# Optimization experiments

Hardware: AMD Instinct MI355X
Metric: run time of the kernel (lower is better)

The kernel has to match this reference:

```python
import jax, jax.numpy as jnp
import numpy as np

J0 = -0.1
J1 = 0.1
ALPHA = 0.15
BUMP_WIDTH_FACTOR = 10.0


def _w_delta7(n):
    idx = jnp.arange(n, dtype=jnp.float32)
    angle_diff = 2.0 * jnp.pi * (idx[:, None] - idx[None, :]) / n
    return jnp.cos(angle_diff)  # [N, N]


def _initial_bump(batch_size, n):
    # initial angle = pi for every batch element (matches r_init=None path)
    angles = jnp.full((batch_size,), jnp.pi, dtype=jnp.float32)
    centers = (angles * n / (2.0 * jnp.pi))[:, None]          # [B, 1]
    width = n / BUMP_WIDTH_FACTOR
    idx = jnp.arange(n, dtype=jnp.float32)[None, :]            # [1, N]
    d = jnp.abs(idx - centers)
    dist = jnp.minimum(d, n - d)                               # circular distance
    bump = jnp.exp(-(dist ** 2) / (2.0 * width ** 2))
    return bump / jnp.linalg.norm(bump, axis=1, keepdims=True)  # [B, N]


def setup_inputs() -> dict:
    key = jax.random.key(0)
    k1, k2, k3 = jax.random.split(key, 3)
    B, S, A, N = 64, 256, 32, 256
    action_signal = jax.random.normal(k1, (B, S, A), dtype=jnp.float32)
    Wo = jax.random.normal(k2, (N, N), dtype=jnp.float32) / np.sqrt(N)
    Wa = jax.random.normal(k3, (A, N, N), dtype=jnp.float32) / np.sqrt(N)
    return {"action_signal": action_signal, "Wo": Wo, "Wa": Wa}


def reference(action_signal, Wo, Wa):
    B, S, A = action_signal.shape
    N = Wo.shape[0]
    W_delta7 = _w_delta7(N)
    r0 = _initial_bump(B, N)
    # static part of the effective weight matrix: J1*W_delta7 + Wo
    W_static = J1 * W_delta7 + Wo  # [N, N]

    def step(r, a_t):
        # a_t: [B, A], r: [B, N]
        # W_eff = J0 + W_static + sum_a a_t[a]*Wa[a]; rec = W_eff @ r (per batch)
        Wa_weighted = jnp.einsum('ba,anm->bnm', a_t, Wa)       # [B, N, N]
        rec = (J0 * jnp.sum(r, axis=-1, keepdims=True)
               + r @ W_static.T
               + jnp.einsum('bnm,bm->bn', Wa_weighted, r))      # [B, N]
        r_new = (1.0 - ALPHA) * r + ALPHA * jax.nn.relu(rec)
        return r_new, r_new

    _, bumps = jax.lax.scan(step, r0, jnp.swapaxes(action_signal, 0, 1))
    bump_history = jnp.swapaxes(bumps, 0, 1)                   # [B, S, N]
    r_delta7 = bump_history @ W_delta7                          # [B, S, N]
    r_history = r_delta7 / jnp.max(r_delta7, axis=2, keepdims=True)
    return r_history, bump_history
```

## Files before the change

### kernel.cpp

```cpp
#include <hip/hip_runtime.h>
#include <math.h>

#define N_    256
#define B_    64
#define S_    256
#define A_    32
#define NSZ   8
#define BSZ   8
#define AROWS 33
#define LROWS 18
#define RROWS 15
#define ATS   12
#define J0_   (-0.1f)
#define J1_   (0.1f)
#define ALPHA_ 0.15f
#define WIDTH_ 25.6f
#define TWO_PI 6.283185307179586f

#define RPAR      (BSZ * N_)
#define RGRP      (2 * RPAR)
#define FLAG_OFF  (8 * RGRP)

#define WA_LDS_FLOATS (NSZ * LROWS * N_)
#define AT_LDS_FLOATS (2 * AROWS * ATS)
#define RLDS_FLOATS   (RPAR)
#define LDS_BYTES ((WA_LDS_FLOATS + AT_LDS_FLOATS + RLDS_FLOATS) * 4)

#define NN ((size_t)N_ * N_)

#define LOADX4_COH(dst, p) \
  asm volatile("global_load_dwordx4 %0, %1, off sc0 sc1" \
               : "=v"(dst) : "v"(p) : "memory")
#define LOADX4(dst, p) \
  asm volatile("global_load_dwordx4 %0, %1, off" : "=v"(dst) : "v"(p) : "memory")
#define WAIT_VM0() asm volatile("s_waitcnt vmcnt(0)" ::: "memory")

#define ROWFMA(wvec, a_idx) do {                                              \
    const float* atp_ = atb + (a_idx) * ATS;                                  \
    const float4 t0_ = *reinterpret_cast<const float4*>(atp_);                \
    const float4 t1_ = *reinterpret_cast<const float4*>(atp_ + 4);            \
    const float at8_[8] = {t0_.x,t0_.y,t0_.z,t0_.w,t1_.x,t1_.y,t1_.z,t1_.w};  \
    _Pragma("unroll")                                                         \
    for (int b_ = 0; b_ < 8; ++b_) {                                          \
      const float dd_ = (wvec).x*rr[b_][0] + (wvec).y*rr[b_][1] +             \
                        (wvec).z*rr[b_][2] + (wvec).w*rr[b_][3];              \
      acc[b_] += at8_[b_] * dd_;                                              \
    }                                                                         \
  } while (0)

__device__ __forceinline__ float bumpval(float idx) {
  float d = fabsf(idx - 128.0f);
  d = fminf(d, 256.0f - d);
  return expf(-d * d / (2.0f * WIDTH_ * WIDTH_));
}

__global__ __launch_bounds__(512, 1)
void ring_scan_kernel(const float* __restrict__ action,
                      const float* __restrict__ Wo,
                      const float* __restrict__ Wa,
                      float* __restrict__ out,
                      float* __restrict__ rws)
{
  extern __shared__ float lds[];
  float* wa_lds = lds;
  float* at_lds = lds + WA_LDS_FLOATS;
  float* r_lds  = lds + WA_LDS_FLOATS + AT_LDS_FLOATS;

  const int tid  = threadIdx.x;
  const int bid  = blockIdx.x;
  const int grp  = bid & 7;
  const int rank = bid >> 3;
  const int b0   = grp * BSZ;
  const int n0   = rank * NSZ;
  float*    rbase = rws + grp * RGRP;
  unsigned* flags = reinterpret_cast<unsigned*>(rws + FLAG_OFF) + grp * 32;

  for (int c = tid; c < NSZ * LROWS * (N_ / 4); c += 512) {
    const int rl = c >> 6;
    const int q  = c & 63;
    const int nl = rl / LROWS;
    const int a  = rl - nl * LROWS;
    const int n  = n0 + nl;
    float4 v;
    if (a < 17) {
      v = *reinterpret_cast<const float4*>(Wa + ((size_t)a * N_ + n) * N_ + q * 4);
    } else {
      const float4 wo = *reinterpret_cast<const float4*>(Wo + (size_t)n * N_ + q * 4);
      const float* wof = reinterpret_cast<const float*>(&wo);
      float tmp[4];
#pragma unroll
      for (int j = 0; j < 4; ++j) {
        const int m = q * 4 + j;
        tmp[j] = J0_ + J1_ * cosf((float)(n - m) * (TWO_PI / N_)) + wof[j];
      }
      v = make_float4(tmp[0], tmp[1], tmp[2], tmp[3]);
    }
    *reinterpret_cast<float4*>(wa_lds + rl * N_ + q * 4) = v;
  }
  if (tid < 16)
    at_lds[(tid >> 3) * (AROWS * ATS) + A_ * ATS + (tid & 7)] = 1.0f;
  if (tid < 256) {
    const int b = tid >> 5, a = tid & 31;
    at_lds[a * ATS + b] = action[((size_t)(b0 + b) * S_) * A_ + a];
  }

  const int wv = tid >> 6;
  const int mq = tid & 63;
  const int nG = n0 + wv;
  const float* wrow = wa_lds + wv * (LROWS * N_);
  const size_t bump_base = (size_t)B_ * S_ * N_;

  float4 sw0,sw1,sw2,sw3,sw4,sw5,sw6,sw7,sw8,sw9,sw10,sw11,sw12,sw13,sw14;
  {
    const float* wg = Wa + ((size_t)17 * N_ + nG) * N_ + mq * 4;
    LOADX4(sw0,  wg);           LOADX4(sw1,  wg + 1*NN);
    LOADX4(sw2,  wg + 2*NN);    LOADX4(sw3,  wg + 3*NN);
    LOADX4(sw4,  wg + 4*NN);    LOADX4(sw5,  wg + 5*NN);
    LOADX4(sw6,  wg + 6*NN);    LOADX4(sw7,  wg + 7*NN);
    LOADX4(sw8,  wg + 8*NN);    LOADX4(sw9,  wg + 9*NN);
    LOADX4(sw10, wg + 10*NN);   LOADX4(sw11, wg + 11*NN);
    LOADX4(sw12, wg + 12*NN);   LOADX4(sw13, wg + 13*NN);
    LOADX4(sw14, wg + 14*NN);
  }

  float g[4]; float ss = 0.0f;
#pragma unroll
  for (int j = 0; j < 4; ++j) { g[j] = bumpval((float)(mq * 4 + j)); ss += g[j] * g[j]; }
#pragma unroll
  for (int off = 1; off < 64; off <<= 1) ss += __shfl_xor(ss, off, 64);
  const float inv_norm = 1.0f / sqrtf(ss);

  float rr[8][4];
#pragma unroll
  for (int b = 0; b < 8; ++b)
#pragma unroll
    for (int j = 0; j < 4; ++j) rr[b][j] = g[j] * inv_norm;
  float rprev = (mq < 8) ? bumpval((float)nG) * inv_norm : 0.0f;

  __syncthreads();
  WAIT_VM0();

  for (int t = 0; t < S_; ++t) {
    const float* atb = at_lds + (t & 1) * (AROWS * ATS);

    if (t > 0) {
      const float* rsrc = rbase + ((t - 1) & 1) * RPAR;
      float4 rq;
      LOADX4_COH(rq, rsrc + tid * 4);
      WAIT_VM0();
      __builtin_amdgcn_sched_barrier(0);
      *reinterpret_cast<float4*>(r_lds + tid * 4) = rq;
      __syncthreads();
#pragma unroll
      for (int b = 0; b < 8; ++b) {
        const float4 rb = *reinterpret_cast<const float4*>(r_lds + b * N_ + mq * 4);
        rr[b][0] = rb.x; rr[b][1] = rb.y; rr[b][2] = rb.z; rr[b][3] = rb.w;
      }
    }

    float acc[8];
#pragma unroll
    for (int b = 0; b < 8; ++b) acc[b] = 0.0f;

#pragma unroll
    for (int a = 0; a < LROWS; ++a) {
      const float4 w = *reinterpret_cast<const float4*>(wrow + a * N_ + mq * 4);
      ROWFMA(w, (a < 17) ? a : 32);
    }
    ROWFMA(sw0, 17);  ROWFMA(sw1, 18);  ROWFMA(sw2, 19);  ROWFMA(sw3, 20);
    ROWFMA(sw4, 21);  ROWFMA(sw5, 22);  ROWFMA(sw6, 23);  ROWFMA(sw7, 24);
    ROWFMA(sw8, 25);  ROWFMA(sw9, 26);  ROWFMA(sw10, 27); ROWFMA(sw11, 28);
    ROWFMA(sw12, 29); ROWFMA(sw13, 30); ROWFMA(sw14, 31);

    const int bit0 = mq & 1, bit1 = mq & 2, bit2 = mq & 4;
    float t0 = bit0 ? acc[1] : acc[0], s0 = bit0 ? acc[0] : acc[1];
    float t1 = bit0 ? acc[3] : acc[2], s1 = bit0 ? acc[2] : acc[3];
    float t2 = bit0 ? acc[5] : acc[4], s2 = bit0 ? acc[4] : acc[5];
    float t3 = bit0 ? acc[7] : acc[6], s3 = bit0 ? acc[6] : acc[7];
    const float u0 = t0 + __shfl_xor(s0, 1, 64);
    const float u1 = t1 + __shfl_xor(s1, 1, 64);
    const float u2 = t2 + __shfl_xor(s2, 1, 64);
    const float u3 = t3 + __shfl_xor(s3, 1, 64);
    const float p0 = bit1 ? u1 : u0, q0 = bit1 ? u0 : u1;
    const float p1 = bit1 ? u3 : u2, q1 = bit1 ? u2 : u3;
    const float m0 = p0 + __shfl_xor(q0, 2, 64);
    const float m1 = p1 + __shfl_xor(q1, 2, 64);
    const float f0 = bit2 ? m1 : m0, g0 = bit2 ? m0 : m1;
    float f = f0 + __shfl_xor(g0, 4, 64);
    f += __shfl_xor(f, 8, 64);
    f += __shfl_xor(f, 16, 64);
    f += __shfl_xor(f, 32, 64);

    float rnew = 0.0f;
    if (mq < 8) {
      rnew = (1.0f - ALPHA_) * rprev + ALPHA_ * fmaxf(f, 0.0f);
      rprev = rnew;
      __hip_atomic_store(rbase + (t & 1) * RPAR + mq * N_ + nG, rnew,
                         __ATOMIC_RELAXED, __HIP_MEMORY_SCOPE_AGENT);
    }

    if (t == S_ - 1) {
      if (mq < 8)
        out[bump_base + ((size_t)(b0 + mq) * S_ + t) * N_ + nG] = rnew;
      break;
    }

    WAIT_VM0();
    __syncthreads();
    if (tid == 0)
      __hip_atomic_store(&flags[rank], (unsigned)(t + 1),
                         __ATOMIC_RELAXED, __HIP_MEMORY_SCOPE_AGENT);

    if (mq < 8)
      out[bump_base + ((size_t)(b0 + mq) * S_ + t) * N_ + nG] = rnew;
    if (tid < 256) {
      const int b = tid >> 5, a = tid & 31;
      at_lds[((t + 1) & 1) * (AROWS * ATS) + a * ATS + b] =
          action[((size_t)(b0 + b) * S_ + (t + 1)) * A_ + a];
    }

    if (wv == 0) {
      const unsigned tgt = (unsigned)(t + 1);
      while (true) {
        const unsigned fl = __hip_atomic_load(&flags[mq & 31], __ATOMIC_RELAXED,
                                              __HIP_MEMORY_SCOPE_AGENT);
        if (__all((int)(fl >= tgt))) break;
        __builtin_amdgcn_s_sleep(1);
      }
    }
    __syncthreads();
  }

  __threadfence();
  __syncthreads();
  if (tid == 0)
    __hip_atomic_store(&flags[rank], 256u, __ATOMIC_RELAXED,
                       __HIP_MEMORY_SCOPE_AGENT);
  if (wv == 0) {
    while (true) {
      const unsigned fl = __hip_atomic_load(&flags[mq & 31], __ATOMIC_RELAXED,
                                            __HIP_MEMORY_SCOPE_AGENT);
      if (__all((int)(fl >= 256u))) break;
      __builtin_amdgcn_s_sleep(1);
    }
  }
  __syncthreads();
  __threadfence();

  float cm[4], sm[4];
#pragma unroll
  for (int j = 0; j < 4; ++j) {
    const float ang = (float)(mq * 4 + j) * (TWO_PI / N_);
    cm[j] = cosf(ang);
    sm[j] = sinf(ang);
  }
  const float* bump = out + bump_base;
  for (int it = 0; it < 8; ++it) {
    const int row_local = rank * 64 + it * 8 + wv;
    const int b = b0 + (row_local >> 8);
    const int s = row_local & 255;
    const size_t row = (size_t)b * S_ + s;
    const float4 v = *reinterpret_cast<const float4*>(bump + row * N_ + mq * 4);
    float C  = cm[0]*v.x + cm[1]*v.y + cm[2]*v.z + cm[3]*v.w;
    float Sv = sm[0]*v.x + sm[1]*v.y + sm[2]*v.z + sm[3]*v.w;
#pragma unroll
    for (int off = 1; off < 64; off <<= 1) {
      C  += __shfl_xor(C,  off, 64);
      Sv += __shfl_xor(Sv, off, 64);
    }
    float y[4];
#pragma unroll
    for (int j = 0; j < 4; ++j) y[j] = cm[j] * C + sm[j] * Sv;
    float mx = fmaxf(fmaxf(y[0], y[1]), fmaxf(y[2], y[3]));
#pragma unroll
    for (int off = 1; off < 64; off <<= 1) mx = fmaxf(mx, __shfl_xor(mx, off, 64));
    const float inv = 1.0f / mx;
    *reinterpret_cast<float4*>(out + row * N_ + mq * 4) =
        make_float4(y[0] * inv, y[1] * inv, y[2] * inv, y[3] * inv);
  }
}

extern "C" void kernel_launch(void* const* d_in, const int* in_sizes, int n_in,
                              void* d_out, int out_size, void* d_ws, size_t ws_size,
                              hipStream_t stream) {
  const float* action = (const float*)d_in[0];
  const float* Wo     = (const float*)d_in[1];
  const float* Wa     = (const float*)d_in[2];
  float* out = (float*)d_out;
  float* rws = (float*)d_ws;

  (void)hipMemsetAsync((char*)d_ws + FLAG_OFF * sizeof(float), 0, 1024, stream);

  (void)hipFuncSetAttribute(reinterpret_cast<const void*>(ring_scan_kernel),
                            hipFuncAttributeMaxDynamicSharedMemorySize, LDS_BYTES);

  void* args[] = {(void*)&action, (void*)&Wo, (void*)&Wa, (void*)&out, (void*)&rws};
  (void)hipLaunchCooperativeKernel(reinterpret_cast<const void*>(ring_scan_kernel),
                                   dim3(256), dim3(512), args,
                                   (unsigned int)LDS_BYTES, stream);
}
```

Before: 1.560 ms.

## Stream action coefficients from global into registers, double-buffered, instead of LDS

Drops the per-step LDS staging of action coefficients. Each thread now loads 8-batch float4 chunks of the action vector straight from global memory into two register buffers, interleaved with the FMA chains, and prefetches the next step's first chunk. It also raises the launch bound to two blocks per CU. This is meant to remove LDS traffic and the staging writes around the barrier, but it adds global loads to the latency-critical recurrence loop and raises register pressure. The tighter launch bound may force spills.

```diff
diff --git a/kernel.cpp b/kernel.cpp
--- a/kernel.cpp
+++ b/kernel.cpp
@@ -5,12 +5,10 @@
 #define B_    64
 #define S_    256
 #define A_    32
+#define SA    (S_ * A_)
 #define NSZ   8
 #define BSZ   8
-#define AROWS 33
 #define LROWS 18
-#define RROWS 15
-#define ATS   12
 #define J0_   (-0.1f)
 #define J1_   (0.1f)
 #define ALPHA_ 0.15f
@@ -22,9 +20,8 @@
 #define FLAG_OFF  (8 * RGRP)
 
 #define WA_LDS_FLOATS (NSZ * LROWS * N_)
-#define AT_LDS_FLOATS (2 * AROWS * ATS)
 #define RLDS_FLOATS   (RPAR)
-#define LDS_BYTES ((WA_LDS_FLOATS + AT_LDS_FLOATS + RLDS_FLOATS) * 4)
+#define LDS_BYTES ((WA_LDS_FLOATS + RLDS_FLOATS) * 4)
 
 #define NN ((size_t)N_ * N_)
 
@@ -35,17 +32,32 @@
   asm volatile("global_load_dwordx4 %0, %1, off" : "=v"(dst) : "v"(p) : "memory")
 #define WAIT_VM0() asm volatile("s_waitcnt vmcnt(0)" ::: "memory")
 
-#define ROWFMA(wvec, a_idx) do {                                              \
-    const float* atp_ = atb + (a_idx) * ATS;                                  \
-    const float4 t0_ = *reinterpret_cast<const float4*>(atp_);                \
-    const float4 t1_ = *reinterpret_cast<const float4*>(atp_ + 4);            \
-    const float at8_[8] = {t0_.x,t0_.y,t0_.z,t0_.w,t1_.x,t1_.y,t1_.z,t1_.w};  \
-    _Pragma("unroll")                                                         \
-    for (int b_ = 0; b_ < 8; ++b_) {                                          \
-      const float dd_ = (wvec).x*rr[b_][0] + (wvec).y*rr[b_][1] +             \
-                        (wvec).z*rr[b_][2] + (wvec).w*rr[b_][3];              \
-      acc[b_] += at8_[b_] * dd_;                                              \
-    }                                                                         \
+#define LW(a) (*reinterpret_cast<const float4*>(wrow + (a) * N_ + mq * 4))
+
+#define LOADCHUNK(dst, base, aoff) do {                      \
+    _Pragma("unroll")                                        \
+    for (int b_ = 0; b_ < 8; ++b_)                           \
+      dst[b_] = *reinterpret_cast<const float4*>(            \
+          (base) + (size_t)b_ * SA + (aoff));                \
+  } while (0)
+
+#define ROWC(wexpr, BUF, comp) do {                               \
+    const float4 w_ = (wexpr);                                    \
+    _Pragma("unroll")                                             \
+    for (int b_ = 0; b_ < 8; ++b_) {                              \
+      const float dd_ = w_.x*rr[b_][0] + w_.y*rr[b_][1] +         \
+                        w_.z*rr[b_][2] + w_.w*rr[b_][3];          \
+      acc[b_] += BUF[b_].comp * dd_;                              \
+    }                                                             \
+  } while (0)
+#define CFMA(w0,w1,w2,w3,BUF) do { ROWC(w0,BUF,x); ROWC(w1,BUF,y); \
+    ROWC(w2,BUF,z); ROWC(w3,BUF,w); } while (0)
+#define ROW1(wexpr) do {                                          \
+    const float4 w_ = (wexpr);                                    \
+    _Pragma("unroll")                                             \
+    for (int b_ = 0; b_ < 8; ++b_)                                \
+      acc[b_] += w_.x*rr[b_][0] + w_.y*rr[b_][1] +                \
+                 w_.z*rr[b_][2] + w_.w*rr[b_][3];                 \
   } while (0)
 
 __device__ __forceinline__ float bumpval(float idx) {
@@ -54,7 +66,7 @@
   return expf(-d * d / (2.0f * WIDTH_ * WIDTH_));
 }
 
-__global__ __launch_bounds__(512, 1)
+__global__ __launch_bounds__(512, 2)
 void ring_scan_kernel(const float* __restrict__ action,
                       const float* __restrict__ Wo,
                       const float* __restrict__ Wa,
@@ -63,8 +75,7 @@
 {
   extern __shared__ float lds[];
   float* wa_lds = lds;
-  float* at_lds = lds + WA_LDS_FLOATS;
-  float* r_lds  = lds + WA_LDS_FLOATS + AT_LDS_FLOATS;
+  float* r_lds  = lds + WA_LDS_FLOATS;
 
   const int tid  = threadIdx.x;
   const int bid  = blockIdx.x;
@@ -97,12 +108,6 @@
     }
     *reinterpret_cast<float4*>(wa_lds + rl * N_ + q * 4) = v;
   }
-  if (tid < 16)
-    at_lds[(tid >> 3) * (AROWS * ATS) + A_ * ATS + (tid & 7)] = 1.0f;
-  if (tid < 256) {
-    const int b = tid >> 5, a = tid & 31;
-    at_lds[a * ATS + b] = action[((size_t)(b0 + b) * S_) * A_ + a];
-  }
 
   const int wv = tid >> 6;
   const int mq = tid & 63;
@@ -140,9 +145,13 @@
   __syncthreads();
   WAIT_VM0();
 
+  float4 atA[8], atB[8];
+  {
+    const float* ab0 = action + (size_t)b0 * SA;
+    LOADCHUNK(atA, ab0, 0);
+  }
+
   for (int t = 0; t < S_; ++t) {
-    const float* atb = at_lds + (t & 1) * (AROWS * ATS);
-
     if (t > 0) {
       const float* rsrc = rbase + ((t - 1) & 1) * RPAR;
       float4 rq;
@@ -158,19 +167,31 @@
       }
     }
 
+    const float* ab  = action + (size_t)b0 * SA + (size_t)t * A_;
+    const float* abn = action + (size_t)b0 * SA +
+                       (size_t)((t < S_ - 1) ? t + 1 : t) * A_;
+
     float acc[8];
 #pragma unroll
     for (int b = 0; b < 8; ++b) acc[b] = 0.0f;
 
-#pragma unroll
-    for (int a = 0; a < LROWS; ++a) {
-      const float4 w = *reinterpret_cast<const float4*>(wrow + a * N_ + mq * 4);
-      ROWFMA(w, (a < 17) ? a : 32);
-    }
-    ROWFMA(sw0, 17);  ROWFMA(sw1, 18);  ROWFMA(sw2, 19);  ROWFMA(sw3, 20);
-    ROWFMA(sw4, 21);  ROWFMA(sw5, 22);  ROWFMA(sw6, 23);  ROWFMA(sw7, 24);
-    ROWFMA(sw8, 25);  ROWFMA(sw9, 26);  ROWFMA(sw10, 27); ROWFMA(sw11, 28);
-    ROWFMA(sw12, 29); ROWFMA(sw13, 30); ROWFMA(sw14, 31);
+    LOADCHUNK(atB, ab, 4);
+    CFMA(LW(0),  LW(1),  LW(2),  LW(3),  atA);
+    LOADCHUNK(atA, ab, 8);
+    CFMA(LW(4),  LW(5),  LW(6),  LW(7),  atB);
+    LOADCHUNK(atB, ab, 12);
+    CFMA(LW(8),  LW(9),  LW(10), LW(11), atA);
+    LOADCHUNK(atA, ab, 16);
+    CFMA(LW(12), LW(13), LW(14), LW(15), atB);
+    LOADCHUNK(atB, ab, 20);
+    CFMA(LW(16), sw0,    sw1,    sw2,    atA);
+    LOADCHUNK(atA, ab, 24);
+    CFMA(sw3,    sw4,    sw5,    sw6,    atB);
+    LOADCHUNK(atB, ab, 28);
+    CFMA(sw7,    sw8,    sw9,    sw10,   atA);
+    LOADCHUNK(atA, abn, 0);
+    CFMA(sw11,   sw12,   sw13,   sw14,   atB);
+    ROW1(LW(17));
 
     const int bit0 = mq & 1, bit1 = mq & 2, bit2 = mq & 4;
     float t0 = bit0 ? acc[1] : acc[0], s0 = bit0 ? acc[0] : acc[1];
@@ -213,11 +234,6 @@
 
     if (mq < 8)
       out[bump_base + ((size_t)(b0 + mq) * S_ + t) * N_ + nG] = rnew;
-    if (tid < 256) {
-      const int b = tid >> 5, a = tid & 31;
-      at_lds[((t + 1) & 1) * (AROWS * ATS) + a * ATS + b] =
-          action[((size_t)(b0 + b) * S_ + (t + 1)) * A_ + a];
-    }
 
     if (wv == 0) {
       const unsigned tgt = (unsigned)(t + 1);
```

Result: slower. 3.077 ms (+97.2%).

## Repartition scan into 4 batch groups of 16 with all weights in LDS

Applied to the files above, without the earlier changes.

Changes the work split from 8 batch groups × 32 blocks (8 neurons, 8 batches each) to 4 batch groups × 64 blocks (4 neurons, 16 batches), with each wave handling half the batch for one neuron. All 33 weight rows per neuron now fit in LDS, so the 15 register-resident weight rows and their global preloads are dropped. The aim is to reuse each weight row across more batch elements and free registers. In exchange, each barrier group now spans 64 blocks instead of 32, which may make the cross-block flag synchronisation at every timestep slower, and each block reads twice as much recurrent state per step.

```diff
diff --git a/kernel.cpp b/kernel.cpp
--- a/kernel.cpp
+++ b/kernel.cpp
@@ -5,12 +5,10 @@
 #define B_    64
 #define S_    256
 #define A_    32
-#define NSZ   8
-#define BSZ   8
+#define SA    (S_ * A_)
+#define NSZ   4
+#define BSZ   16
 #define AROWS 33
-#define LROWS 18
-#define RROWS 15
-#define ATS   12
 #define J0_   (-0.1f)
 #define J1_   (0.1f)
 #define ALPHA_ 0.15f
@@ -19,33 +17,29 @@
 
 #define RPAR      (BSZ * N_)
 #define RGRP      (2 * RPAR)
-#define FLAG_OFF  (8 * RGRP)
-
-#define WA_LDS_FLOATS (NSZ * LROWS * N_)
-#define AT_LDS_FLOATS (2 * AROWS * ATS)
+#define FLAG_OFF  (4 * RGRP)
+
+#define WA_LDS_FLOATS (NSZ * AROWS * N_)
+#define AT_LDS_FLOATS (2 * A_ * BSZ)
 #define RLDS_FLOATS   (RPAR)
 #define LDS_BYTES ((WA_LDS_FLOATS + AT_LDS_FLOATS + RLDS_FLOATS) * 4)
-
-#define NN ((size_t)N_ * N_)
 
 #define LOADX4_COH(dst, p) \
   asm volatile("global_load_dwordx4 %0, %1, off sc0 sc1" \
                : "=v"(dst) : "v"(p) : "memory")
-#define LOADX4(dst, p) \
-  asm volatile("global_load_dwordx4 %0, %1, off" : "=v"(dst) : "v"(p) : "memory")
 #define WAIT_VM0() asm volatile("s_waitcnt vmcnt(0)" ::: "memory")
 
-#define ROWFMA(wvec, a_idx) do {                                              \
-    const float* atp_ = atb + (a_idx) * ATS;                                  \
-    const float4 t0_ = *reinterpret_cast<const float4*>(atp_);                \
-    const float4 t1_ = *reinterpret_cast<const float4*>(atp_ + 4);            \
-    const float at8_[8] = {t0_.x,t0_.y,t0_.z,t0_.w,t1_.x,t1_.y,t1_.z,t1_.w};  \
-    _Pragma("unroll")                                                         \
-    for (int b_ = 0; b_ < 8; ++b_) {                                          \
-      const float dd_ = (wvec).x*rr[b_][0] + (wvec).y*rr[b_][1] +             \
-                        (wvec).z*rr[b_][2] + (wvec).w*rr[b_][3];              \
-      acc[b_] += at8_[b_] * dd_;                                              \
-    }                                                                         \
+#define LW(a) (*reinterpret_cast<const float4*>(wrow + (a) * N_ + mq * 4))
+
+#define ACC1(i, atv) \
+  acc[i] += (atv) * (w_.x*rr[i][0] + w_.y*rr[i][1] + w_.z*rr[i][2] + w_.w*rr[i][3])
+
+#define ROWFMA(a) do {                                                        \
+    const float4 w_  = LW(a);                                                 \
+    const float4 ta_ = *reinterpret_cast<const float4*>(atbh + (a)*BSZ);      \
+    const float4 tb_ = *reinterpret_cast<const float4*>(atbh + (a)*BSZ + 4);  \
+    ACC1(0, ta_.x); ACC1(1, ta_.y); ACC1(2, ta_.z); ACC1(3, ta_.w);           \
+    ACC1(4, tb_.x); ACC1(5, tb_.y); ACC1(6, tb_.z); ACC1(7, tb_.w);           \
   } while (0)
 
 __device__ __forceinline__ float bumpval(float idx) {
@@ -68,21 +62,21 @@
 
   const int tid  = threadIdx.x;
   const int bid  = blockIdx.x;
-  const int grp  = bid & 7;
-  const int rank = bid >> 3;
+  const int grp  = bid & 3;
+  const int rank = bid >> 2;
   const int b0   = grp * BSZ;
   const int n0   = rank * NSZ;
   float*    rbase = rws + grp * RGRP;
-  unsigned* flags = reinterpret_cast<unsigned*>(rws + FLAG_OFF) + grp * 32;
-
-  for (int c = tid; c < NSZ * LROWS * (N_ / 4); c += 512) {
+  unsigned* flags = reinterpret_cast<unsigned*>(rws + FLAG_OFF) + grp * 64;
+
+  for (int c = tid; c < NSZ * AROWS * (N_ / 4); c += 512) {
     const int rl = c >> 6;
     const int q  = c & 63;
-    const int nl = rl / LROWS;
-    const int a  = rl - nl * LROWS;
+    const int nl = rl / AROWS;
+    const int a  = rl - nl * AROWS;
     const int n  = n0 + nl;
     float4 v;
-    if (a < 17) {
+    if (a < A_) {
       v = *reinterpret_cast<const float4*>(Wa + ((size_t)a * N_ + n) * N_ + q * 4);
     } else {
       const float4 wo = *reinterpret_cast<const float4*>(Wo + (size_t)n * N_ + q * 4);
@@ -97,31 +91,18 @@
     }
     *reinterpret_cast<float4*>(wa_lds + rl * N_ + q * 4) = v;
   }
-  if (tid < 16)
-    at_lds[(tid >> 3) * (AROWS * ATS) + A_ * ATS + (tid & 7)] = 1.0f;
-  if (tid < 256) {
-    const int b = tid >> 5, a = tid & 31;
-    at_lds[a * ATS + b] = action[((size_t)(b0 + b) * S_) * A_ + a];
-  }
-
-  const int wv = tid >> 6;
-  const int mq = tid & 63;
-  const int nG = n0 + wv;
-  const float* wrow = wa_lds + wv * (LROWS * N_);
+  {
+    const int a = tid & 31, b = tid >> 5;
+    at_lds[a * BSZ + b] = action[(size_t)(b0 + b) * SA + a];
+  }
+
+  const int wv    = tid >> 6;
+  const int mq    = tid & 63;
+  const int nloc  = wv & 3;
+  const int nG    = n0 + nloc;
+  const int bhalf = (wv >> 2) * 8;
+  const float* wrow = wa_lds + nloc * (AROWS * N_);
   const size_t bump_base = (size_t)B_ * S_ * N_;
-
-  float4 sw0,sw1,sw2,sw3,sw4,sw5,sw6,sw7,sw8,sw9,sw10,sw11,sw12,sw13,sw14;
-  {
-    const float* wg = Wa + ((size_t)17 * N_ + nG) * N_ + mq * 4;
-    LOADX4(sw0,  wg);           LOADX4(sw1,  wg + 1*NN);
-    LOADX4(sw2,  wg + 2*NN);    LOADX4(sw3,  wg + 3*NN);
-    LOADX4(sw4,  wg + 4*NN);    LOADX4(sw5,  wg + 5*NN);
-    LOADX4(sw6,  wg + 6*NN);    LOADX4(sw7,  wg + 7*NN);
-    LOADX4(sw8,  wg + 8*NN);    LOADX4(sw9,  wg + 9*NN);
-    LOADX4(sw10, wg + 10*NN);   LOADX4(sw11, wg + 11*NN);
-    LOADX4(sw12, wg + 12*NN);   LOADX4(sw13, wg + 13*NN);
-    LOADX4(sw14, wg + 14*NN);
-  }
 
   float g[4]; float ss = 0.0f;
 #pragma unroll
@@ -138,22 +119,24 @@
   float rprev = (mq < 8) ? bumpval((float)nG) * inv_norm : 0.0f;
 
   __syncthreads();
-  WAIT_VM0();
 
   for (int t = 0; t < S_; ++t) {
-    const float* atb = at_lds + (t & 1) * (AROWS * ATS);
+    const float* atbh = at_lds + (t & 1) * (A_ * BSZ) + bhalf;
 
     if (t > 0) {
       const float* rsrc = rbase + ((t - 1) & 1) * RPAR;
-      float4 rq;
-      LOADX4_COH(rq, rsrc + tid * 4);
+      float4 rq0, rq1;
+      LOADX4_COH(rq0, rsrc + tid * 8);
+      LOADX4_COH(rq1, rsrc + tid * 8 + 4);
       WAIT_VM0();
       __builtin_amdgcn_sched_barrier(0);
-      *reinterpret_cast<float4*>(r_lds + tid * 4) = rq;
+      *reinterpret_cast<float4*>(r_lds + tid * 8)     = rq0;
+      *reinterpret_cast<float4*>(r_lds + tid * 8 + 4) = rq1;
       __syncthreads();
 #pragma unroll
       for (int b = 0; b < 8; ++b) {
-        const float4 rb = *reinterpret_cast<const float4*>(r_lds + b * N_ + mq * 4);
+        const float4 rb =
+            *reinterpret_cast<const float4*>(r_lds + (bhalf + b) * N_ + mq * 4);
         rr[b][0] = rb.x; rr[b][1] = rb.y; rr[b][2] = rb.z; rr[b][3] = rb.w;
       }
     }
@@ -163,14 +146,13 @@
     for (int b = 0; b < 8; ++b) acc[b] = 0.0f;
 
 #pragma unroll
-    for (int a = 0; a < LROWS; ++a) {
-      const float4 w = *reinterpret_cast<const float4*>(wrow + a * N_ + mq * 4);
-      ROWFMA(w, (a < 17) ? a : 32);
-    }
-    ROWFMA(sw0, 17);  ROWFMA(sw1, 18);  ROWFMA(sw2, 19);  ROWFMA(sw3, 20);
-    ROWFMA(sw4, 21);  ROWFMA(sw5, 22);  ROWFMA(sw6, 23);  ROWFMA(sw7, 24);
-    ROWFMA(sw8, 25);  ROWFMA(sw9, 26);  ROWFMA(sw10, 27); ROWFMA(sw11, 28);
-    ROWFMA(sw12, 29); ROWFMA(sw13, 30); ROWFMA(sw14, 31);
+    for (int a = 0; a < A_; ++a) ROWFMA(a);
+    {
+      const float4 w_ = LW(A_);
+#pragma unroll
+      for (int b = 0; b < 8; ++b)
+        acc[b] += w_.x*rr[b][0] + w_.y*rr[b][1] + w_.z*rr[b][2] + w_.w*rr[b][3];
+    }
 
     const int bit0 = mq & 1, bit1 = mq & 2, bit2 = mq & 4;
     float t0 = bit0 ? acc[1] : acc[0], s0 = bit0 ? acc[0] : acc[1];
@@ -195,13 +177,13 @@
     if (mq < 8) {
       rnew = (1.0f - ALPHA_) * rprev + ALPHA_ * fmaxf(f, 0.0f);
       rprev = rnew;
-      __hip_atomic_store(rbase + (t & 1) * RPAR + mq * N_ + nG, rnew,
+      __hip_atomic_store(rbase + (t & 1) * RPAR + (bhalf + mq) * N_ + nG, rnew,
                          __ATOMIC_RELAXED, __HIP_MEMORY_SCOPE_AGENT);
     }
 
     if (t == S_ - 1) {
       if (mq < 8)
-        out[bump_base + ((size_t)(b0 + mq) * S_ + t) * N_ + nG] = rnew;
+        out[bump_base + ((size_t)(b0 + bhalf + mq) * S_ + t) * N_ + nG] = rnew;
       break;
     }
 
@@ -212,17 +194,17 @@
                          __ATOMIC_RELAXED, __HIP_MEMORY_SCOPE_AGENT);
 
     if (mq < 8)
-      out[bump_base + ((size_t)(b0 + mq) * S_ + t) * N_ + nG] = rnew;
-    if (tid < 256) {
-      const int b = tid >> 5, a = tid & 31;
-      at_lds[((t + 1) & 1) * (AROWS * ATS) + a * ATS + b] =
-          action[((size_t)(b0 + b) * S_ + (t + 1)) * A_ + a];
+      out[bump_base + ((size_t)(b0 + bhalf + mq) * S_ + t) * N_ + nG] = rnew;
+    {
+      const int a = tid & 31, b = tid >> 5;
+      at_lds[((t + 1) & 1) * (A_ * BSZ) + a * BSZ + b] =
+          action[(size_t)(b0 + b) * SA + (size_t)(t + 1) * A_ + a];
     }
 
     if (wv == 0) {
       const unsigned tgt = (unsigned)(t + 1);
       while (true) {
-        const unsigned fl = __hip_atomic_load(&flags[mq & 31], __ATOMIC_RELAXED,
+        const unsigned fl = __hip_atomic_load(&flags[mq], __ATOMIC_RELAXED,
                                               __HIP_MEMORY_SCOPE_AGENT);
         if (__all((int)(fl >= tgt))) break;
         __builtin_amdgcn_s_sleep(1);
@@ -238,7 +220,7 @@
                        __HIP_MEMORY_SCOPE_AGENT);
   if (wv == 0) {
     while (true) {
-      const unsigned fl = __hip_atomic_load(&flags[mq & 31], __ATOMIC_RELAXED,
+      const unsigned fl = __hip_atomic_load(&flags[mq], __ATOMIC_RELAXED,
                                             __HIP_MEMORY_SCOPE_AGENT);
       if (__all((int)(fl >= 256u))) break;
       __builtin_amdgcn_s_sleep(1);
```

Measured after the change: 1.907 ms. +22.2%, slower.
